# Performance work log

Measured on AMD Instinct MI355X. Metric: run time of the kernel, lower is better.

The kernel has to match this reference:

```python
import jax, jax.numpy as jnp
import numpy as np

HEAD_SIZE = 64
EMBED_DIM = 1024
SEQ_LEN = 4096
BATCH = 4


def setup_inputs() -> dict:
    key = jax.random.key(0)
    kx, kk, kq, kv = jax.random.split(key, 4)
    x = jax.random.normal(kx, (BATCH, SEQ_LEN, EMBED_DIM), dtype=jnp.float32)
    # nn.Linear(embedding_dim, head_size, bias=False): weight [head_size, embed];
    # store transposed [embed, head_size] so projection is x @ W.
    scale = 1.0 / np.sqrt(EMBED_DIM)
    Wk = jax.random.uniform(kk, (EMBED_DIM, HEAD_SIZE), jnp.float32, -scale, scale)
    Wq = jax.random.uniform(kq, (EMBED_DIM, HEAD_SIZE), jnp.float32, -scale, scale)
    Wv = jax.random.uniform(kv, (EMBED_DIM, HEAD_SIZE), jnp.float32, -scale, scale)
    return {"x": x, "Wk": Wk, "Wq": Wq, "Wv": Wv}


def reference(x, Wk, Wq, Wv):
    B, T, C = x.shape
    k = x @ Wk  # [B, T, H]
    q = x @ Wq  # [B, T, H]
    v = x @ Wv  # [B, T, H]
    H = k.shape[-1]
    s = jnp.einsum('bth,bsh->bts', q, k) * (H ** -0.5)  # [B, T, T]
    causal = jnp.tril(jnp.ones((T, T), dtype=bool))
    s = jnp.where(causal, s, -jnp.inf)
    a = jax.nn.softmax(s, axis=-1)  # dropout p=0.0 -> identity
    z = jnp.einsum('bts,bsh->bth', a, v)  # [B, T, H]
    return z
```

## Files before the change

### kernel.cpp

```cpp
#include <hip/hip_runtime.h>

#define SEQ 4096
#define EMB 1024
#define HS 64

typedef __attribute__((ext_vector_type(8))) short bf16x8;
typedef __attribute__((ext_vector_type(4))) float f32x4;

__device__ __forceinline__ unsigned short f2b(float f) {
    union { float f; unsigned u; } v; v.f = f;
    unsigned r = v.u + 0x7fffu + ((v.u >> 16) & 1u);
    return (unsigned short)(r >> 16);
}
__device__ __forceinline__ float b2f(unsigned short h) {
    union { unsigned u; float f; } v; v.u = ((unsigned)h) << 16;
    return v.f;
}
template <typename T>
__device__ __forceinline__ void gll16(const T* g, void* l) {
    __builtin_amdgcn_global_load_lds(
        (const __attribute__((address_space(1))) unsigned int*)(g),
        (__attribute__((address_space(3))) unsigned int*)(l), 16, 0, 0);
}

__global__ __launch_bounds__(256) void wt_kernel(const float* __restrict__ Wq,
                                                 const float* __restrict__ Wk,
                                                 const float* __restrict__ Wv,
                                                 unsigned short* __restrict__ Wt) {
    int id = blockIdx.x * 256 + threadIdx.x;
    int mat = id >> 16;
    int rem = id & 65535;
    int k = rem >> 6;
    int n = rem & 63;
    const float* W = (mat == 0) ? Wq : (mat == 1) ? Wk : Wv;
    float scale = (mat == 0) ? 0.125f * 1.44269504f : 1.0f;
    Wt[(mat * HS + n) * EMB + k] = f2b(W[k * HS + n] * scale);
}

__global__ __launch_bounds__(256, 2) void proj_kernel(const float* __restrict__ x,
                                                      const unsigned short* __restrict__ Wt,
                                                      unsigned short* __restrict__ Qb,
                                                      unsigned short* __restrict__ Kb,
                                                      unsigned short* __restrict__ Vt) {
    __shared__ float xf[2][32 * 64];
    __shared__ unsigned short wb[2][192 * 64];
    const int tid = threadIdx.x;
    const int wave = tid >> 6, lane = tid & 63;
    const int col = lane & 15, quad = lane >> 4;
    const int m0 = blockIdx.x * 32;
    const int b = m0 >> 12, t0 = m0 & 4095;

    const int xr_in = lane >> 4;
    const int xc = lane & 15;
    const int wr_in = lane >> 3;
    const int wc = lane & 7;

    f32x4 acc[2][3];
    #pragma unroll
    for (int i = 0; i < 2; i++)
        #pragma unroll
        for (int j = 0; j < 3; j++) acc[i][j] = (f32x4){0.f, 0.f, 0.f, 0.f};

    auto stage = [&](int k0, int bufi) {
        #pragma unroll
        for (int t = 0; t < 2; t++) {
            int R = (wave + t * 4) * 4;
            int row = R + xr_in;
            gll16(x + (size_t)(m0 + row) * EMB + k0 + ((xc ^ (row & 15)) << 2),
                  &xf[bufi][R * 64]);
        }
        #pragma unroll
        for (int t = 0; t < 6; t++) {
            int R = (wave * 6 + t) * 8;
            int row = R + wr_in;
            gll16(Wt + (size_t)row * EMB + k0 + ((wc ^ (row & 7)) << 3),
                  &wb[bufi][R * 64]);
        }
    };

    stage(0, 0);
    int buf = 0;
    #pragma unroll 1
    for (int k0 = 0; k0 < EMB; k0 += 64) {
        __syncthreads();
        if (k0 + 64 < EMB) stage(k0 + 64, buf ^ 1);
        #pragma unroll
        for (int kc = 0; kc < 2; kc++) {
            const int q2 = quad + kc * 4;
            bf16x8 af[2], bfr[3];
            #pragma unroll
            for (int mt = 0; mt < 2; mt++) {
                int rr = mt * 16 + col;
                float4 lo = *(const float4*)&xf[buf][rr * 64 + (((2 * q2) ^ col) << 2)];
                float4 hi = *(const float4*)&xf[buf][rr * 64 + (((2 * q2 + 1) ^ col) << 2)];
                bf16x8 a;
                a[0] = (short)f2b(lo.x); a[1] = (short)f2b(lo.y);
                a[2] = (short)f2b(lo.z); a[3] = (short)f2b(lo.w);
                a[4] = (short)f2b(hi.x); a[5] = (short)f2b(hi.y);
                a[6] = (short)f2b(hi.z); a[7] = (short)f2b(hi.w);
                af[mt] = a;
            }
            #pragma unroll
            for (int nt = 0; nt < 3; nt++) {
                int rn = wave * 48 + nt * 16 + col;
                bfr[nt] = *(const bf16x8*)&wb[buf][rn * 64 + ((q2 ^ (col & 7)) << 3)];
            }
            #pragma unroll
            for (int mt = 0; mt < 2; mt++)
                #pragma unroll
                for (int nt = 0; nt < 3; nt++)
                    acc[mt][nt] = __builtin_amdgcn_mfma_f32_16x16x32_bf16(af[mt], bfr[nt], acc[mt][nt], 0, 0, 0);
        }
        buf ^= 1;
    }

    #pragma unroll
    for (int mt = 0; mt < 2; mt++)
        #pragma unroll
        for (int nt = 0; nt < 3; nt++) {
            const int g = wave * 3 + nt;
            const int mat = g >> 2;
            const int ncol = (g & 3) * 16 + col;
            #pragma unroll
            for (int r = 0; r < 4; r++) {
                unsigned short val = f2b(acc[mt][nt][r]);
                int row = mt * 16 + quad * 4 + r;
                if (mat == 0)      Qb[(size_t)(m0 + row) * HS + ncol] = val;
                else if (mat == 1) Kb[(size_t)(m0 + row) * HS + ncol] = val;
                else               Vt[((size_t)b * HS + ncol) * SEQ + t0 + row] = val;
            }
        }
}

__global__ __launch_bounds__(512, 4) void attn_kernel(const unsigned short* __restrict__ Qb,
                                                      const unsigned short* __restrict__ Kb,
                                                      const unsigned short* __restrict__ Vt,
                                                      unsigned short* __restrict__ Opart,
                                                      float* __restrict__ Lpart,
                                                      float* __restrict__ out) {
    __shared__ unsigned short Kl[3][64 * 64];
    __shared__ unsigned short Vl[3][64 * 64];
    __shared__ unsigned short P_lds[8][16 * 72];
    const int tid = threadIdx.x;
    const int wave = tid >> 6, lane = tid & 63;
    const int col = lane & 15, quad = lane >> 4;
    const int bid = blockIdx.x;
    const int g = 118 - (bid >> 2);
    const int b = bid & 3;
    int T = 0, accp = 0;
    for (;;) { int np = T / 5 + 1; if (accp + np > g) break; accp += np; T++; }
    const int piece = g - accp;
    const int np = T / 5 + 1;
    const int q0 = T << 7;
    const int s_beg = piece * 10;
    const int s_end = min(s_beg + 10, 2 * T + 2);

    const unsigned short* Kp = Kb + ((size_t)(b << 12)) * HS;
    const unsigned short* Vp = Vt + (size_t)b * HS * SEQ;

    bf16x8 qf[2];
    #pragma unroll
    for (int c = 0; c < 2; c++)
        qf[c] = *(const bf16x8*)(Qb + ((size_t)(b << 12) + q0 + wave * 16 + col) * HS + quad * 8 + c * 32);

    f32x4 o[4];
    float l[4];
    #pragma unroll
    for (int ct = 0; ct < 4; ct++) o[ct] = (f32x4){0.f, 0.f, 0.f, 0.f};
    #pragma unroll
    for (int r = 0; r < 4; r++) l[r] = 0.f;

    const int r_in = lane >> 3;
    const int ch = lane & 7;

    auto stage = [&](int s, int bufi) {
        const int kv0 = s << 6;
        int R = wave * 8;
        int row = R + r_in;
        gll16(Kp + (size_t)(kv0 + row) * HS + ((ch ^ (row & 7)) << 3), &Kl[bufi][R * 64]);
        gll16(Vp + (size_t)row * SEQ + kv0 + ((ch ^ (row & 7)) << 3), &Vl[bufi][R * 64]);
    };

    stage(s_beg, 0);
    stage(min(s_beg + 1, s_end - 1), 1);
    int bufr = 0;
    const int grb = (b << 12) + q0 + wave * 16;
    const int rgb = q0 + wave * 16 + quad * 4;
    unsigned short* Pl = P_lds[wave];

    #pragma unroll 1
    for (int s = s_beg; s < s_end; s++) {
        asm volatile("s_waitcnt vmcnt(2)\n\ts_barrier" ::: "memory");
        stage(min(s + 2, s_end - 1), (bufr + 2) % 3);
        const int kv0 = s << 6;

        f32x4 sacc[4];
        #pragma unroll
        for (int ct = 0; ct < 4; ct++) sacc[ct] = (f32x4){0.f, 0.f, 0.f, 0.f};
        #pragma unroll
        for (int ct = 0; ct < 4; ct++) {
            int n = ct * 16 + col;
            #pragma unroll
            for (int kc = 0; kc < 2; kc++) {
                bf16x8 kf = *(const bf16x8*)&Kl[bufr][n * 64 + (((kc * 4 + quad) ^ (col & 7)) << 3)];
                sacc[ct] = __builtin_amdgcn_mfma_f32_16x16x32_bf16(qf[kc], kf, sacc[ct], 0, 0, 0);
            }
        }

        float p[4][4];
        #pragma unroll
        for (int ct = 0; ct < 4; ct++) {
            int cg = kv0 + ct * 16 + col;
            #pragma unroll
            for (int r = 0; r < 4; r++) {
                float e = __builtin_exp2f(sacc[ct][r]);
                e = (cg > rgb + r) ? 0.f : e;
                p[ct][r] = e;
                l[r] += e;
            }
        }

        #pragma unroll
        for (int ct = 0; ct < 4; ct++)
            #pragma unroll
            for (int r = 0; r < 4; r++)
                Pl[(quad * 4 + r) * 72 + ct * 16 + col] = f2b(p[ct][r]);
        bf16x8 pf[2];
        #pragma unroll
        for (int c = 0; c < 2; c++)
            pf[c] = *(const bf16x8*)&Pl[col * 72 + quad * 8 + c * 32];

        #pragma unroll
        for (int ct = 0; ct < 4; ct++) {
            int h = ct * 16 + col;
            #pragma unroll
            for (int kc = 0; kc < 2; kc++) {
                bf16x8 vf = *(const bf16x8*)&Vl[bufr][h * 64 + (((kc * 4 + quad) ^ (col & 7)) << 3)];
                o[ct] = __builtin_amdgcn_mfma_f32_16x16x32_bf16(pf[kc], vf, o[ct], 0, 0, 0);
            }
        }
        bufr = (bufr == 2) ? 0 : bufr + 1;
    }

    #pragma unroll
    for (int off = 1; off < 16; off <<= 1)
        #pragma unroll
        for (int r = 0; r < 4; r++)
            l[r] += __shfl_xor(l[r], off, 64);

    if (np == 1) {
        #pragma unroll
        for (int ct = 0; ct < 4; ct++)
            #pragma unroll
            for (int r = 0; r < 4; r++)
                out[(size_t)(grb + quad * 4 + r) * HS + ct * 16 + col] = o[ct][r] / l[r];
    } else {
        const int widx = bid * 8 + wave;
        unsigned short* Op = Opart + (size_t)widx * 1024;
        #pragma unroll
        for (int ct = 0; ct < 4; ct++) {
            ushort4 st;
            st.x = f2b(o[ct][0]); st.y = f2b(o[ct][1]);
            st.z = f2b(o[ct][2]); st.w = f2b(o[ct][3]);
            *(ushort4*)(Op + ct * 256 + lane * 4) = st;
        }
        if (col == 0) {
            #pragma unroll
            for (int r = 0; r < 4; r++)
                Lpart[widx * 16 + quad * 4 + r] = l[r];
        }
    }
}

__global__ __launch_bounds__(256) void comb_kernel(const unsigned short* __restrict__ Opart,
                                                   const float* __restrict__ Lpart,
                                                   float* __restrict__ out) {
    const int bid = blockIdx.x;
    const int b = bid & 3;
    const int idx = bid >> 2;
    const int T = 5 + (idx % 27);
    const int wave = idx / 27;
    const int tid = threadIdx.x;
    const int lane = tid & 63, ct = tid >> 6;
    const int col = lane & 15, quad = lane >> 4;

    const int q = T / 5, r5 = T % 5;
    const int base = T + 5 * q * (q - 1) / 2 + r5 * q;
    const int np = q + 1;

    float acc[4] = {0.f, 0.f, 0.f, 0.f};
    float l[4] = {0.f, 0.f, 0.f, 0.f};
    for (int p = 0; p < np; p++) {
        int gg = base + p;
        int bidp = ((118 - gg) << 2) | b;
        int widx = bidp * 8 + wave;
        ushort4 v = *(const ushort4*)(Opart + (size_t)widx * 1024 + ct * 256 + lane * 4);
        acc[0] += b2f(v.x); acc[1] += b2f(v.y);
        acc[2] += b2f(v.z); acc[3] += b2f(v.w);
        #pragma unroll
        for (int r = 0; r < 4; r++)
            l[r] += Lpart[widx * 16 + quad * 4 + r];
    }
    const size_t rowb = (size_t)(b << 12) + (T << 7) + wave * 16 + quad * 4;
    #pragma unroll
    for (int r = 0; r < 4; r++)
        out[(rowb + r) * HS + ct * 16 + col] = acc[r] / l[r];
}

extern "C" void kernel_launch(void* const* d_in, const int* in_sizes, int n_in,
                              void* d_out, int out_size, void* d_ws, size_t ws_size,
                              hipStream_t stream) {
    const float* x  = (const float*)d_in[0];
    const float* Wk = (const float*)d_in[1];
    const float* Wq = (const float*)d_in[2];
    const float* Wv = (const float*)d_in[3];
    float* out = (float*)d_out;

    char* ws = (char*)d_ws;
    unsigned short* Wt = (unsigned short*)(ws);
    unsigned short* Qb = (unsigned short*)(ws + 393216);
    unsigned short* Kb = (unsigned short*)(ws + 2490368);
    unsigned short* Vt = (unsigned short*)(ws + 4587520);
    unsigned short* Opart = (unsigned short*)(ws + 6684672);
    float* Lpart          = (float*)(ws + 14483456);

    wt_kernel<<<dim3(768), dim3(256), 0, stream>>>(Wq, Wk, Wv, Wt);
    proj_kernel<<<dim3(512), dim3(256), 0, stream>>>(x, Wt, Qb, Kb, Vt);
    attn_kernel<<<dim3(476), dim3(512), 0, stream>>>(Qb, Kb, Vt, Opart, Lpart, out);
    comb_kernel<<<dim3(864), dim3(256), 0, stream>>>(Opart, Lpart, out);
}
```

Baseline: 147.5 us.

## Compute transposed QK^T so P stays in registers, dropping the LDS round-trip

Swaps the MFMA operand order so the score tile comes out transposed, with each lane holding four consecutive KV positions for one query. That layout matches the A-operand layout of the PV MFMA, so probabilities are packed to bf16 with v_cvt_pk_bf16_f32 and fed directly, removing the per-tile P write/read through LDS. V fragments are now gathered as two 4-element LDS reads to match the new k ordering. Row sums become one scalar per lane, reduced across quads and redistributed with shuffles at the end. The cost is twice as many, narrower V loads from LDS.

```diff
diff --git a/kernel.cpp b/kernel.cpp
--- a/kernel.cpp
+++ b/kernel.cpp
@@ -5,6 +5,7 @@
 #define HS 64
 
 typedef __attribute__((ext_vector_type(8))) short bf16x8;
+typedef __attribute__((ext_vector_type(4))) short bf16x4;
 typedef __attribute__((ext_vector_type(4))) float f32x4;
 
 __device__ __forceinline__ unsigned short f2b(float f) {
@@ -15,6 +16,11 @@
 __device__ __forceinline__ float b2f(unsigned short h) {
     union { unsigned u; float f; } v; v.u = ((unsigned)h) << 16;
     return v.f;
+}
+__device__ __forceinline__ unsigned cvtpk(float a, float b) {
+    unsigned r;
+    asm("v_cvt_pk_bf16_f32 %0, %1, %2" : "=v"(r) : "v"(a), "v"(b));
+    return r;
 }
 template <typename T>
 __device__ __forceinline__ void gll16(const T* g, void* l) {
@@ -140,7 +146,6 @@
                                                       float* __restrict__ out) {
     __shared__ unsigned short Kl[3][64 * 64];
     __shared__ unsigned short Vl[3][64 * 64];
-    __shared__ unsigned short P_lds[8][16 * 72];
     const int tid = threadIdx.x;
     const int wave = tid >> 6, lane = tid & 63;
     const int col = lane & 15, quad = lane >> 4;
@@ -164,11 +169,9 @@
         qf[c] = *(const bf16x8*)(Qb + ((size_t)(b << 12) + q0 + wave * 16 + col) * HS + quad * 8 + c * 32);
 
     f32x4 o[4];
-    float l[4];
+    float l = 0.f;
     #pragma unroll
     for (int ct = 0; ct < 4; ct++) o[ct] = (f32x4){0.f, 0.f, 0.f, 0.f};
-    #pragma unroll
-    for (int r = 0; r < 4; r++) l[r] = 0.f;
 
     const int r_in = lane >> 3;
     const int ch = lane & 7;
@@ -185,8 +188,7 @@
     stage(min(s_beg + 1, s_end - 1), 1);
     int bufr = 0;
     const int grb = (b << 12) + q0 + wave * 16;
-    const int rgb = q0 + wave * 16 + quad * 4;
-    unsigned short* Pl = P_lds[wave];
+    const int qg = q0 + wave * 16 + col;
 
     #pragma unroll 1
     for (int s = s_beg; s < s_end; s++) {
@@ -203,57 +205,62 @@
             #pragma unroll
             for (int kc = 0; kc < 2; kc++) {
                 bf16x8 kf = *(const bf16x8*)&Kl[bufr][n * 64 + (((kc * 4 + quad) ^ (col & 7)) << 3)];
-                sacc[ct] = __builtin_amdgcn_mfma_f32_16x16x32_bf16(qf[kc], kf, sacc[ct], 0, 0, 0);
+                sacc[ct] = __builtin_amdgcn_mfma_f32_16x16x32_bf16(kf, qf[kc], sacc[ct], 0, 0, 0);
             }
         }
 
         float p[4][4];
         #pragma unroll
         for (int ct = 0; ct < 4; ct++) {
-            int cg = kv0 + ct * 16 + col;
+            int kvb = kv0 + ct * 16 + quad * 4;
             #pragma unroll
             for (int r = 0; r < 4; r++) {
                 float e = __builtin_exp2f(sacc[ct][r]);
-                e = (cg > rgb + r) ? 0.f : e;
+                e = (kvb + r > qg) ? 0.f : e;
                 p[ct][r] = e;
-                l[r] += e;
-            }
-        }
-
-        #pragma unroll
-        for (int ct = 0; ct < 4; ct++)
-            #pragma unroll
-            for (int r = 0; r < 4; r++)
-                Pl[(quad * 4 + r) * 72 + ct * 16 + col] = f2b(p[ct][r]);
+                l += e;
+            }
+        }
+
         bf16x8 pf[2];
         #pragma unroll
-        for (int c = 0; c < 2; c++)
-            pf[c] = *(const bf16x8*)&Pl[col * 72 + quad * 8 + c * 32];
+        for (int kc = 0; kc < 2; kc++) {
+            union { unsigned u[4]; bf16x8 v; } pu;
+            pu.u[0] = cvtpk(p[2 * kc][0],     p[2 * kc][1]);
+            pu.u[1] = cvtpk(p[2 * kc][2],     p[2 * kc][3]);
+            pu.u[2] = cvtpk(p[2 * kc + 1][0], p[2 * kc + 1][1]);
+            pu.u[3] = cvtpk(p[2 * kc + 1][2], p[2 * kc + 1][3]);
+            pf[kc] = pu.v;
+        }
 
         #pragma unroll
         for (int ct = 0; ct < 4; ct++) {
-            int h = ct * 16 + col;
+            const unsigned short* Vrow = &Vl[bufr][(ct * 16 + col) * 64];
             #pragma unroll
             for (int kc = 0; kc < 2; kc++) {
-                bf16x8 vf = *(const bf16x8*)&Vl[bufr][h * 64 + (((kc * 4 + quad) ^ (col & 7)) << 3)];
+                int c0 = ((kc << 2) + (quad >> 1)) ^ (col & 7);
+                int c1 = ((kc << 2) + 2 + (quad >> 1)) ^ (col & 7);
+                bf16x4 lo = *(const bf16x4*)&Vrow[(c0 << 3) + ((quad & 1) << 2)];
+                bf16x4 hi = *(const bf16x4*)&Vrow[(c1 << 3) + ((quad & 1) << 2)];
+                bf16x8 vf = __builtin_shufflevector(lo, hi, 0, 1, 2, 3, 4, 5, 6, 7);
                 o[ct] = __builtin_amdgcn_mfma_f32_16x16x32_bf16(pf[kc], vf, o[ct], 0, 0, 0);
             }
         }
         bufr = (bufr == 2) ? 0 : bufr + 1;
     }
 
-    #pragma unroll
-    for (int off = 1; off < 16; off <<= 1)
-        #pragma unroll
-        for (int r = 0; r < 4; r++)
-            l[r] += __shfl_xor(l[r], off, 64);
+    l += __shfl_xor(l, 16, 64);
+    l += __shfl_xor(l, 32, 64);
 
     if (np == 1) {
+        float lq[4];
+        #pragma unroll
+        for (int r = 0; r < 4; r++) lq[r] = __shfl(l, quad * 4 + r, 64);
         #pragma unroll
         for (int ct = 0; ct < 4; ct++)
             #pragma unroll
             for (int r = 0; r < 4; r++)
-                out[(size_t)(grb + quad * 4 + r) * HS + ct * 16 + col] = o[ct][r] / l[r];
+                out[(size_t)(grb + quad * 4 + r) * HS + ct * 16 + col] = o[ct][r] / lq[r];
     } else {
         const int widx = bid * 8 + wave;
         unsigned short* Op = Opart + (size_t)widx * 1024;
@@ -264,11 +271,7 @@
             st.z = f2b(o[ct][2]); st.w = f2b(o[ct][3]);
             *(ushort4*)(Op + ct * 256 + lane * 4) = st;
         }
-        if (col == 0) {
-            #pragma unroll
-            for (int r = 0; r < 4; r++)
-                Lpart[widx * 16 + quad * 4 + r] = l[r];
-        }
+        if (quad == 0) Lpart[widx * 16 + col] = l;
     }
 }
 
```

Result: no change. 146.9 us (-0.4%).
